# Optimization experiments

Measured on AMD Instinct MI355X. Metric: run time of the kernel, lower is better.

Reference implementation:

```python
import jax, jax.numpy as jnp
import numpy as np

N = 50000        # nodes
E = 800000       # edges
F_IN = 128       # num_features
H = 256          # hidden_dim
B = 128          # number of graphs (batch_size)
NUM_CLASSES = 10
SCALE = 3        # (r-1)*Lev+1 = 3
NNZ = 1200000    # nnz of multiscale wavelet transform matrix [SCALE*N, N]


def setup_inputs() -> dict:
    key = jax.random.key(0)
    ks = jax.random.split(key, 16)
    x = jax.random.normal(ks[0], (N, F_IN), jnp.float32)
    edge_index = jax.random.randint(ks[1], (2, E), 0, N)
    batch = jnp.sort(jax.random.randint(ks[2], (N,), 0, B))
    d = jax.random.normal(ks[3], (NNZ,), jnp.float32) * 0.1
    rows = jax.random.randint(ks[4], (NNZ,), 0, SCALE * N)
    cols = jax.random.randint(ks[5], (NNZ,), 0, N)
    d_index = jnp.stack([rows, cols])

    def lin(k, fi, fo):
        return jax.random.normal(k, (fi, fo), jnp.float32) * (1.0 / np.sqrt(fi))

    return {
        "x": x,
        "W1": lin(ks[6], F_IN, H), "b1": jnp.zeros((H,), jnp.float32),
        "W2": lin(ks[7], H, H),    "b2": jnp.zeros((H,), jnp.float32),
        "W3": lin(ks[8], H, H),    "b3": jnp.zeros((H,), jnp.float32),
        "fc1_w": lin(ks[9], SCALE * H, H),  "fc1_b": jnp.zeros((H,), jnp.float32),
        "fc2_w": lin(ks[10], H, H // 2),    "fc2_b": jnp.zeros((H // 2,), jnp.float32),
        "fc3_w": lin(ks[11], H // 2, NUM_CLASSES), "fc3_b": jnp.zeros((NUM_CLASSES,), jnp.float32),
        "d": d,
        "edge_index": edge_index,
        "batch": batch,
        "d_index": d_index,
    }


def reference(x, W1, b1, W2, b2, W3, b3, fc1_w, fc1_b, fc2_w, fc2_b,
              fc3_w, fc3_b, d, edge_index, batch, d_index):
    # --- GCN normalization (PyG GCNConv: add self-loops, sym norm) ---
    loops = jnp.arange(N, dtype=edge_index.dtype)
    src = jnp.concatenate([edge_index[0], loops])
    dst = jnp.concatenate([edge_index[1], loops])
    deg = jax.ops.segment_sum(jnp.ones_like(src, jnp.float32), dst, num_segments=N)
    dinv = jax.lax.rsqrt(jnp.maximum(deg, 1.0))  # deg >= 1 due to self-loops
    norm = dinv[src] * dinv[dst]                 # [E+N]

    def gcn(h, W, b):
        m = h @ W                                              # [N, H]
        agg = jax.ops.segment_sum(norm[:, None] * m[src], dst, num_segments=N)
        return agg + b

    h = jax.nn.relu(gcn(x, W1, b1))
    h = jax.nn.relu(gcn(h, W2, b2))
    h = jax.nn.relu(gcn(h, W3, b3))

    # --- MultiScale wavelet transform + per-graph pooling ---
    # sparse [SCALE*N, N] matmul: xt = T @ h
    xt = jax.ops.segment_sum(d[:, None] * h[d_index[1]], d_index[0],
                             num_segments=SCALE * N)           # [SCALE*N, H]
    # pool per (scale, graph): segment id = scale*B + graph_id
    seg = (jnp.arange(SCALE)[:, None] * B + batch[None, :]).reshape(-1)
    pooled = jax.ops.segment_sum(xt, seg, num_segments=SCALE * B)
    pooled = pooled.reshape(SCALE, B, H).transpose(1, 0, 2).reshape(B, SCALE * H)

    # --- FC head (dropout is identity in eval) ---
    z = jax.nn.relu(pooled @ fc1_w + fc1_b)
    z = jax.nn.relu(z @ fc2_w + fc2_b)
    return jax.nn.log_softmax(z @ fc3_w + fc3_b, axis=-1)      # [B, NUM_CLASSES]
```

## Files before the change

### kernel.cpp

```cpp
#include <hip/hip_runtime.h>
#include <hip/hip_bf16.h>

#define GN 50000
#define GE 800000
#define FIN 128
#define GH 256
#define GB 128
#define NCLS 10
#define GSCALE 3
#define GNNZ 1200000
#define NSEG (GSCALE * GB)
#define PAD 16

__global__ __launch_bounds__(256) void deg_count_kernel(const int* __restrict__ dst,
                                                        int* __restrict__ deg) {
  int i = blockIdx.x * 256 + threadIdx.x;
  if (i < GE) atomicAdd(&deg[dst[i]], 1);
}

__global__ __launch_bounds__(256) void dinv_kernel(const int* __restrict__ deg,
                                                   float* __restrict__ dinv) {
  int i = blockIdx.x * 256 + threadIdx.x;
  if (i < GN) dinv[i] = 1.0f / sqrtf((float)(deg[i] + 1));
}

__global__ __launch_bounds__(256) void scan1_kernel(const int* __restrict__ in,
                                                    int* __restrict__ out,
                                                    int* __restrict__ btot, int n) {
  __shared__ int sh[256];
  int b = blockIdx.x, tid = threadIdx.x;
  int i = b * 256 + tid;
  int v = (i < n) ? in[i] : 0;
  sh[tid] = v;
  __syncthreads();
  for (int ofs = 1; ofs < 256; ofs <<= 1) {
    int t = (tid >= ofs) ? sh[tid - ofs] : 0;
    __syncthreads();
    sh[tid] += t;
    __syncthreads();
  }
  if (i < n) out[i] = sh[tid] - v;
  if (tid == 255) btot[b] = sh[255];
}

__global__ __launch_bounds__(256) void scan2_kernel(int* __restrict__ btot, int nb) {
  __shared__ int sh[256];
  int tid = threadIdx.x;
  int v = (tid < nb) ? btot[tid] : 0;
  sh[tid] = v;
  __syncthreads();
  for (int ofs = 1; ofs < 256; ofs <<= 1) {
    int t = (tid >= ofs) ? sh[tid - ofs] : 0;
    __syncthreads();
    sh[tid] += t;
    __syncthreads();
  }
  if (tid < nb) btot[tid] = sh[tid] - v;
}

__global__ __launch_bounds__(256) void scan3_kernel(int* __restrict__ out,
                                                    const int* __restrict__ btot,
                                                    int n, int total) {
  int b = blockIdx.x, tid = threadIdx.x;
  int i = b * 256 + tid;
  if (i < n) out[i] += btot[b];
  if (i == 0) out[n] = total;
}

__global__ __launch_bounds__(256) void exscan_strided_kernel(const int* __restrict__ in,
                                                             int* __restrict__ out,
                                                             int n, int stride) {
  __shared__ int sh[256];
  __shared__ int carry;
  int tid = threadIdx.x;
  if (tid == 0) carry = 0;
  __syncthreads();
  for (int base = 0; base < n; base += 256) {
    int i = base + tid;
    int v = (i < n) ? in[(size_t)i * stride] : 0;
    sh[tid] = v;
    __syncthreads();
    for (int ofs = 1; ofs < 256; ofs <<= 1) {
      int t = (tid >= ofs) ? sh[tid - ofs] : 0;
      __syncthreads();
      sh[tid] += t;
      __syncthreads();
    }
    if (i < n) out[i] = carry + sh[tid] - v;
    int total = sh[255];
    __syncthreads();
    if (tid == 0) carry += total;
    __syncthreads();
  }
  if (tid == 0) out[n] = carry;
}

__global__ __launch_bounds__(256) void csr_fill_kernel(const int* __restrict__ src,
                                                       const int* __restrict__ dst,
                                                       int* __restrict__ cur,
                                                       int* __restrict__ csr_src) {
  int i = blockIdx.x * 256 + threadIdx.x;
  if (i < GE) {
    int j = atomicAdd(&cur[dst[i]], 1);
    csr_src[j] = src[i];
  }
}

__device__ __forceinline__ int seg_of(int row, const int* __restrict__ batch) {
  int sc = row / GN;
  int node = row - sc * GN;
  return sc * GB + batch[node];
}

__global__ __launch_bounds__(256) void seg_cnt_kernel(const int* __restrict__ rows,
                                                      const int* __restrict__ batch,
                                                      int* __restrict__ scnt_p) {
  int i = blockIdx.x * 256 + threadIdx.x;
  if (i < GNNZ) atomicAdd(&scnt_p[(size_t)seg_of(rows[i], batch) * PAD], 1);
}

__global__ __launch_bounds__(256) void scur_init_kernel(const int* __restrict__ soff,
                                                        int* __restrict__ scur_p) {
  int s = blockIdx.x * 256 + threadIdx.x;
  if (s < NSEG) scur_p[(size_t)s * PAD] = soff[s];
}

__global__ __launch_bounds__(256) void seg_fill_kernel(const int* __restrict__ rows,
                                                       const int* __restrict__ cols,
                                                       const float* __restrict__ d,
                                                       const int* __restrict__ batch,
                                                       int* __restrict__ scur_p,
                                                       int* __restrict__ scol,
                                                       float* __restrict__ sd) {
  int i = blockIdx.x * 256 + threadIdx.x;
  if (i < GNNZ) {
    int j = atomicAdd(&scur_p[(size_t)seg_of(rows[i], batch) * PAD], 1);
    scol[j] = cols[i];
    sd[j] = d[i];
  }
}

template <int K>
__global__ __launch_bounds__(256) void gemm_kernel(const float* __restrict__ A,
                                                   const float* __restrict__ W,
                                                   float* __restrict__ C, int M) {
  __shared__ float As[16][64];
  __shared__ float Bs[16][64];
  int tid = threadIdx.x;
  int col0 = blockIdx.x * 64;
  int row0 = blockIdx.y * 64;
  float acc[4][4] = {};
  int ar = tid >> 2, akq = tid & 3;
  int bkr = tid >> 4, bcq = tid & 15;
  int ty = tid >> 4, tx = tid & 15;
  for (int kk = 0; kk < K; kk += 16) {
    int arow = row0 + ar;
    if (arow >= M) arow = M - 1;
    float4 av = *(const float4*)&A[(size_t)arow * K + kk + akq * 4];
    float4 bv = *(const float4*)&W[(size_t)(kk + bkr) * GH + col0 + bcq * 4];
    __syncthreads();
    As[akq * 4 + 0][ar] = av.x;
    As[akq * 4 + 1][ar] = av.y;
    As[akq * 4 + 2][ar] = av.z;
    As[akq * 4 + 3][ar] = av.w;
    *(float4*)&Bs[bkr][bcq * 4] = bv;
    __syncthreads();
#pragma unroll
    for (int k = 0; k < 16; ++k) {
      float4 a = *(const float4*)&As[k][ty * 4];
      float4 b = *(const float4*)&Bs[k][tx * 4];
      acc[0][0] += a.x * b.x; acc[0][1] += a.x * b.y; acc[0][2] += a.x * b.z; acc[0][3] += a.x * b.w;
      acc[1][0] += a.y * b.x; acc[1][1] += a.y * b.y; acc[1][2] += a.y * b.z; acc[1][3] += a.y * b.w;
      acc[2][0] += a.z * b.x; acc[2][1] += a.z * b.y; acc[2][2] += a.z * b.z; acc[2][3] += a.z * b.w;
      acc[3][0] += a.w * b.x; acc[3][1] += a.w * b.y; acc[3][2] += a.w * b.z; acc[3][3] += a.w * b.w;
    }
  }
#pragma unroll
  for (int i = 0; i < 4; ++i) {
    int r = row0 + ty * 4 + i;
    if (r < M) {
      float4 v = make_float4(acc[i][0], acc[i][1], acc[i][2], acc[i][3]);
      *(float4*)&C[(size_t)r * GH + col0 + tx * 4] = v;
    }
  }
}

__global__ __launch_bounds__(256) void agg_kernel(const float* __restrict__ m,
                                                  const float* __restrict__ dinv,
                                                  const int* __restrict__ off,
                                                  const int* __restrict__ srcs,
                                                  const float* __restrict__ bias,
                                                  float* __restrict__ out) {
  int node = blockIdx.x * 4 + (threadIdx.x >> 6);
  if (node >= GN) return;
  int lane = threadIdx.x & 63;
  float4 acc = *(const float4*)&bias[lane * 4];
  float di = dinv[node];
  float w0 = di * di;
  float4 mv = *(const float4*)&m[(size_t)node * GH + lane * 4];
  acc.x += w0 * mv.x; acc.y += w0 * mv.y; acc.z += w0 * mv.z; acc.w += w0 * mv.w;
  int e0 = off[node], e1 = off[node + 1];
  for (int e = e0; e < e1; ++e) {
    int s = srcs[e];
    float w = di * dinv[s];
    float4 v = *(const float4*)&m[(size_t)s * GH + lane * 4];
    acc.x += w * v.x; acc.y += w * v.y; acc.z += w * v.z; acc.w += w * v.w;
  }
  acc.x = fmaxf(acc.x, 0.f); acc.y = fmaxf(acc.y, 0.f);
  acc.z = fmaxf(acc.z, 0.f); acc.w = fmaxf(acc.w, 0.f);
  *(float4*)&out[(size_t)node * GH + lane * 4] = acc;
}

__global__ __launch_bounds__(256) void pooled_kernel(const float* __restrict__ h,
                                                     const int* __restrict__ soff,
                                                     const int* __restrict__ scol,
                                                     const float* __restrict__ sd,
                                                     float* __restrict__ pooled) {
  __shared__ int lcol[256];
  __shared__ float ld[256];
  int seg = blockIdx.x;
  int j0 = soff[seg], j1 = soff[seg + 1];
  int cnt = j1 - j0;
  int nparts = gridDim.y;
  int per = (cnt + nparts - 1) / nparts;
  int s = j0 + blockIdx.y * per;
  int e = s + per;
  if (e > j1) e = j1;
  int tid = threadIdx.x;
  float acc = 0.f;
  for (int base = s; base < e; base += 256) {
    int nload = e - base;
    if (nload > 256) nload = 256;
    __syncthreads();
    if (tid < nload) {
      lcol[tid] = scol[base + tid];
      ld[tid] = sd[base + tid];
    }
    __syncthreads();
    for (int t = 0; t < nload; ++t) {
      acc += ld[t] * h[(size_t)lcol[t] * GH + tid];
    }
  }
  atomicAdd(&pooled[(size_t)seg * GH + tid], acc);
}

__global__ __launch_bounds__(256) void fc1_kernel(const float* __restrict__ pooled,
                                                  const float* __restrict__ w,
                                                  const float* __restrict__ b,
                                                  float* __restrict__ z1) {
  __shared__ float vin[GSCALE * GH];
  int g = blockIdx.x, tid = threadIdx.x;
#pragma unroll
  for (int it = 0; it < GSCALE; ++it)
    vin[it * GH + tid] = pooled[(size_t)(it * GB + g) * GH + tid];
  __syncthreads();
  float acc = b[tid];
  for (int j = 0; j < GSCALE * GH; ++j) acc += vin[j] * w[(size_t)j * GH + tid];
  z1[(size_t)g * GH + tid] = fmaxf(acc, 0.f);
}

__global__ __launch_bounds__(128) void fc2_kernel(const float* __restrict__ z1,
                                                  const float* __restrict__ w,
                                                  const float* __restrict__ b,
                                                  float* __restrict__ z2) {
  __shared__ float vin[GH];
  int g = blockIdx.x, tid = threadIdx.x;
  vin[tid] = z1[(size_t)g * GH + tid];
  vin[128 + tid] = z1[(size_t)g * GH + 128 + tid];
  __syncthreads();
  float acc = b[tid];
  for (int j = 0; j < GH; ++j) acc += vin[j] * w[(size_t)j * 128 + tid];
  z2[(size_t)g * 128 + tid] = fmaxf(acc, 0.f);
}

__global__ __launch_bounds__(128) void fc3_kernel(const float* __restrict__ z2,
                                                  const float* __restrict__ w,
                                                  const float* __restrict__ b,
                                                  float* __restrict__ out) {
  int g = threadIdx.x;
  float logit[NCLS];
#pragma unroll
  for (int o = 0; o < NCLS; ++o) logit[o] = b[o];
  for (int k = 0; k < 128; ++k) {
    float zv = z2[(size_t)g * 128 + k];
#pragma unroll
    for (int o = 0; o < NCLS; ++o) logit[o] += zv * w[k * NCLS + o];
  }
  float mx = logit[0];
#pragma unroll
  for (int o = 1; o < NCLS; ++o) mx = fmaxf(mx, logit[o]);
  float lse = 0.f;
#pragma unroll
  for (int o = 0; o < NCLS; ++o) lse += expf(logit[o] - mx);
  lse = logf(lse);
#pragma unroll
  for (int o = 0; o < NCLS; ++o) out[(size_t)g * NCLS + o] = logit[o] - mx - lse;
}

static inline size_t alignup(size_t x) { return (x + 1023) & ~(size_t)1023; }

extern "C" void kernel_launch(void* const* d_in, const int* in_sizes, int n_in,
                              void* d_out, int out_size, void* d_ws, size_t ws_size,
                              hipStream_t stream) {
  const float* x      = (const float*)d_in[0];
  const float* W1     = (const float*)d_in[1];
  const float* b1     = (const float*)d_in[2];
  const float* W2     = (const float*)d_in[3];
  const float* b2     = (const float*)d_in[4];
  const float* W3     = (const float*)d_in[5];
  const float* b3     = (const float*)d_in[6];
  const float* fc1w   = (const float*)d_in[7];
  const float* fc1b   = (const float*)d_in[8];
  const float* fc2w   = (const float*)d_in[9];
  const float* fc2b   = (const float*)d_in[10];
  const float* fc3w   = (const float*)d_in[11];
  const float* fc3b   = (const float*)d_in[12];
  const float* dval   = (const float*)d_in[13];
  const int* eidx     = (const int*)d_in[14];
  const int* batch    = (const int*)d_in[15];
  const int* didx     = (const int*)d_in[16];
  float* out          = (float*)d_out;

  const int* esrc = eidx;
  const int* edst = eidx + GE;
  const int* nzrow = didx;
  const int* nzcol = didx + GNNZ;

  char* ws = (char*)d_ws;
  size_t o = 0;
  auto take = [&](size_t bytes) { char* p = ws + o; o += alignup(bytes); return p; };
  int*   deg     = (int*)take(GN * 4);
  int*   off     = (int*)take((GN + 1) * 4);
  int*   cur     = (int*)take(GN * 4);
  int*   btot    = (int*)take(256 * 4);
  float* dinv    = (float*)take(GN * 4);
  int*   csr_src = (int*)take(GE * 4);
  int*   scnt_p  = (int*)take(NSEG * PAD * 4);
  int*   soff    = (int*)take((NSEG + 1) * 4);
  int*   scur_p  = (int*)take(NSEG * PAD * 4);
  int*   scol    = (int*)take(GNNZ * 4);
  float* sd      = (float*)take(GNNZ * 4);
  float* mbuf    = (float*)take((size_t)GN * GH * 4);
  float* hA      = (float*)take((size_t)GN * GH * 4);
  float* hB      = (float*)take((size_t)GN * GH * 4);
  float* pooled  = (float*)take((size_t)NSEG * GH * 4);
  float* z1      = (float*)take((size_t)GB * GH * 4);
  float* z2      = (float*)take((size_t)GB * 128 * 4);
  (void)ws_size; (void)n_in; (void)in_sizes; (void)out_size;

  const int NB = (GN + 255) / 256;

  hipMemsetAsync(deg, 0, GN * 4, stream);
  hipMemsetAsync(scnt_p, 0, NSEG * PAD * 4, stream);
  hipMemsetAsync(pooled, 0, (size_t)NSEG * GH * 4, stream);

  deg_count_kernel<<<GE / 256, 256, 0, stream>>>(edst, deg);
  dinv_kernel<<<NB, 256, 0, stream>>>(deg, dinv);
  scan1_kernel<<<NB, 256, 0, stream>>>(deg, off, btot, GN);
  scan2_kernel<<<1, 256, 0, stream>>>(btot, NB);
  scan3_kernel<<<NB, 256, 0, stream>>>(off, btot, GN, GE);
  hipMemcpyAsync(cur, off, GN * 4, hipMemcpyDeviceToDevice, stream);
  csr_fill_kernel<<<GE / 256, 256, 0, stream>>>(esrc, edst, cur, csr_src);

  seg_cnt_kernel<<<(GNNZ + 255) / 256, 256, 0, stream>>>(nzrow, batch, scnt_p);
  exscan_strided_kernel<<<1, 256, 0, stream>>>(scnt_p, soff, NSEG, PAD);
  scur_init_kernel<<<(NSEG + 255) / 256, 256, 0, stream>>>(soff, scur_p);
  seg_fill_kernel<<<(GNNZ + 255) / 256, 256, 0, stream>>>(nzrow, nzcol, dval, batch,
                                                          scur_p, scol, sd);

  dim3 ggrid(GH / 64, (GN + 63) / 64);
  gemm_kernel<FIN><<<ggrid, 256, 0, stream>>>(x, W1, mbuf, GN);
  agg_kernel<<<(GN + 3) / 4, 256, 0, stream>>>(mbuf, dinv, off, csr_src, b1, hA);
  gemm_kernel<GH><<<ggrid, 256, 0, stream>>>(hA, W2, mbuf, GN);
  agg_kernel<<<(GN + 3) / 4, 256, 0, stream>>>(mbuf, dinv, off, csr_src, b2, hB);
  gemm_kernel<GH><<<ggrid, 256, 0, stream>>>(hB, W3, mbuf, GN);
  agg_kernel<<<(GN + 3) / 4, 256, 0, stream>>>(mbuf, dinv, off, csr_src, b3, hA);

  pooled_kernel<<<dim3(NSEG, 8), 256, 0, stream>>>(hA, soff, scol, sd, pooled);

  fc1_kernel<<<GB, 256, 0, stream>>>(pooled, fc1w, fc1b, z1);
  fc2_kernel<<<GB, 128, 0, stream>>>(z1, fc2w, fc2b, z2);
  fc3_kernel<<<1, 128, 0, stream>>>(z2, fc3w, fc3b, out);
}
```

Before: 1.152 ms.

## Restructure wavelet pooling as column-sorted scatter into LDS segment accumulators

The sparse wavelet-transform nonzeros are now sorted by column (node) instead of by output segment. Each block owns a node chunk and a 32-wide feature slice, reads each h row slice once, and scatters d*h into a shared-memory accumulator over all 384 segments. Per-chunk partials are written into the reused GEMM buffer and summed by a separate reduction kernel. This replaces the old per-segment gather of random h rows and its contended global atomics, at the cost of LDS atomics and an extra reduction pass. The GCN aggregation loop is also unrolled by two edges to raise memory-level parallelism.

```diff
diff --git a/kernel.cpp b/kernel.cpp
--- a/kernel.cpp
+++ b/kernel.cpp
@@ -10,7 +10,11 @@
 #define GSCALE 3
 #define GNNZ 1200000
 #define NSEG (GSCALE * GB)
-#define PAD 16
+
+#define SLW 32
+#define NSLICE (GH / SLW)
+#define NCHUNK 64
+#define CPC ((GN + NCHUNK - 1) / NCHUNK)
 
 __global__ __launch_bounds__(256) void deg_count_kernel(const int* __restrict__ dst,
                                                         int* __restrict__ deg) {
@@ -67,34 +71,6 @@
   if (i == 0) out[n] = total;
 }
 
-__global__ __launch_bounds__(256) void exscan_strided_kernel(const int* __restrict__ in,
-                                                             int* __restrict__ out,
-                                                             int n, int stride) {
-  __shared__ int sh[256];
-  __shared__ int carry;
-  int tid = threadIdx.x;
-  if (tid == 0) carry = 0;
-  __syncthreads();
-  for (int base = 0; base < n; base += 256) {
-    int i = base + tid;
-    int v = (i < n) ? in[(size_t)i * stride] : 0;
-    sh[tid] = v;
-    __syncthreads();
-    for (int ofs = 1; ofs < 256; ofs <<= 1) {
-      int t = (tid >= ofs) ? sh[tid - ofs] : 0;
-      __syncthreads();
-      sh[tid] += t;
-      __syncthreads();
-    }
-    if (i < n) out[i] = carry + sh[tid] - v;
-    int total = sh[255];
-    __syncthreads();
-    if (tid == 0) carry += total;
-    __syncthreads();
-  }
-  if (tid == 0) out[n] = carry;
-}
-
 __global__ __launch_bounds__(256) void csr_fill_kernel(const int* __restrict__ src,
                                                        const int* __restrict__ dst,
                                                        int* __restrict__ cur,
@@ -112,31 +88,24 @@
   return sc * GB + batch[node];
 }
 
-__global__ __launch_bounds__(256) void seg_cnt_kernel(const int* __restrict__ rows,
-                                                      const int* __restrict__ batch,
-                                                      int* __restrict__ scnt_p) {
-  int i = blockIdx.x * 256 + threadIdx.x;
-  if (i < GNNZ) atomicAdd(&scnt_p[(size_t)seg_of(rows[i], batch) * PAD], 1);
-}
-
-__global__ __launch_bounds__(256) void scur_init_kernel(const int* __restrict__ soff,
-                                                        int* __restrict__ scur_p) {
-  int s = blockIdx.x * 256 + threadIdx.x;
-  if (s < NSEG) scur_p[(size_t)s * PAD] = soff[s];
-}
-
-__global__ __launch_bounds__(256) void seg_fill_kernel(const int* __restrict__ rows,
+__global__ __launch_bounds__(256) void col_cnt_kernel(const int* __restrict__ cols,
+                                                      int* __restrict__ ccnt) {
+  int i = blockIdx.x * 256 + threadIdx.x;
+  if (i < GNNZ) atomicAdd(&ccnt[cols[i]], 1);
+}
+
+__global__ __launch_bounds__(256) void col_fill_kernel(const int* __restrict__ rows,
                                                        const int* __restrict__ cols,
                                                        const float* __restrict__ d,
                                                        const int* __restrict__ batch,
-                                                       int* __restrict__ scur_p,
-                                                       int* __restrict__ scol,
-                                                       float* __restrict__ sd) {
+                                                       int* __restrict__ ccur,
+                                                       int* __restrict__ bseg,
+                                                       float* __restrict__ bd) {
   int i = blockIdx.x * 256 + threadIdx.x;
   if (i < GNNZ) {
-    int j = atomicAdd(&scur_p[(size_t)seg_of(rows[i], batch) * PAD], 1);
-    scol[j] = cols[i];
-    sd[j] = d[i];
+    int j = atomicAdd(&ccur[cols[i]], 1);
+    bseg[j] = seg_of(rows[i], batch);
+    bd[j] = d[i];
   }
 }
 
@@ -200,7 +169,19 @@
   float4 mv = *(const float4*)&m[(size_t)node * GH + lane * 4];
   acc.x += w0 * mv.x; acc.y += w0 * mv.y; acc.z += w0 * mv.z; acc.w += w0 * mv.w;
   int e0 = off[node], e1 = off[node + 1];
-  for (int e = e0; e < e1; ++e) {
+  int e = e0;
+  for (; e + 2 <= e1; e += 2) {
+    int s0 = srcs[e], s1 = srcs[e + 1];
+    float w0a = di * dinv[s0];
+    float w1a = di * dinv[s1];
+    float4 v0 = *(const float4*)&m[(size_t)s0 * GH + lane * 4];
+    float4 v1 = *(const float4*)&m[(size_t)s1 * GH + lane * 4];
+    acc.x += w0a * v0.x + w1a * v1.x;
+    acc.y += w0a * v0.y + w1a * v1.y;
+    acc.z += w0a * v0.z + w1a * v1.z;
+    acc.w += w0a * v0.w + w1a * v1.w;
+  }
+  if (e < e1) {
     int s = srcs[e];
     float w = di * dinv[s];
     float4 v = *(const float4*)&m[(size_t)s * GH + lane * 4];
@@ -211,37 +192,54 @@
   *(float4*)&out[(size_t)node * GH + lane * 4] = acc;
 }
 
-__global__ __launch_bounds__(256) void pooled_kernel(const float* __restrict__ h,
-                                                     const int* __restrict__ soff,
-                                                     const int* __restrict__ scol,
-                                                     const float* __restrict__ sd,
-                                                     float* __restrict__ pooled) {
-  __shared__ int lcol[256];
-  __shared__ float ld[256];
+__global__ __launch_bounds__(256) void pooled2_kernel(const float* __restrict__ h,
+                                                      const int* __restrict__ coff,
+                                                      const int* __restrict__ bseg,
+                                                      const float* __restrict__ bd,
+                                                      float* __restrict__ pp) {
+  __shared__ float acc[NSEG * SLW];
+  int tid = threadIdx.x;
+  int chunk = blockIdx.x, slice = blockIdx.y;
+#pragma unroll
+  for (int t = tid; t < NSEG * SLW; t += 256) acc[t] = 0.f;
+  __syncthreads();
+
+  int wid = tid >> 6;
+  int lane = tid & 63;
+  int sub = lane >> 5;
+  int f = lane & 31;
+  int c0base = chunk * CPC;
+  int cend = c0base + CPC;
+  if (cend > GN) cend = GN;
+  for (int c0 = c0base + wid * 2; c0 < cend; c0 += 8) {
+    int c = c0 + sub;
+    bool valid = c < cend;
+    float hv = valid ? h[(size_t)c * GH + slice * SLW + f] : 0.f;
+    int p0 = valid ? coff[c] : 0;
+    int p1 = valid ? coff[c + 1] : 0;
+    for (int p = p0; p < p1; ++p) {
+      int s = bseg[p];
+      float dv = bd[p];
+      atomicAdd(&acc[s * SLW + f], dv * hv);
+    }
+  }
+  __syncthreads();
+  float* dst = &pp[((size_t)slice * NCHUNK + chunk) * (NSEG * SLW)];
+#pragma unroll
+  for (int t = tid; t < NSEG * SLW; t += 256) dst[t] = acc[t];
+}
+
+__global__ __launch_bounds__(256) void pool_reduce_kernel(const float* __restrict__ pp,
+                                                          float* __restrict__ pooled) {
   int seg = blockIdx.x;
-  int j0 = soff[seg], j1 = soff[seg + 1];
-  int cnt = j1 - j0;
-  int nparts = gridDim.y;
-  int per = (cnt + nparts - 1) / nparts;
-  int s = j0 + blockIdx.y * per;
-  int e = s + per;
-  if (e > j1) e = j1;
   int tid = threadIdx.x;
-  float acc = 0.f;
-  for (int base = s; base < e; base += 256) {
-    int nload = e - base;
-    if (nload > 256) nload = 256;
-    __syncthreads();
-    if (tid < nload) {
-      lcol[tid] = scol[base + tid];
-      ld[tid] = sd[base + tid];
-    }
-    __syncthreads();
-    for (int t = 0; t < nload; ++t) {
-      acc += ld[t] * h[(size_t)lcol[t] * GH + tid];
-    }
-  }
-  atomicAdd(&pooled[(size_t)seg * GH + tid], acc);
+  int slice = tid >> 5;
+  int f = tid & 31;
+  float v = 0.f;
+  for (int ch = 0; ch < NCHUNK; ++ch) {
+    v += pp[((size_t)slice * NCHUNK + ch) * (NSEG * SLW) + seg * SLW + f];
+  }
+  pooled[(size_t)seg * GH + tid] = v;
 }
 
 __global__ __launch_bounds__(256) void fc1_kernel(const float* __restrict__ pooled,
@@ -335,24 +333,24 @@
   int*   btot    = (int*)take(256 * 4);
   float* dinv    = (float*)take(GN * 4);
   int*   csr_src = (int*)take(GE * 4);
-  int*   scnt_p  = (int*)take(NSEG * PAD * 4);
-  int*   soff    = (int*)take((NSEG + 1) * 4);
-  int*   scur_p  = (int*)take(NSEG * PAD * 4);
-  int*   scol    = (int*)take(GNNZ * 4);
-  float* sd      = (float*)take(GNNZ * 4);
+  int*   ccnt    = (int*)take(GN * 4);
+  int*   coff    = (int*)take((GN + 1) * 4);
+  int*   ccur    = (int*)take(GN * 4);
+  int*   bseg    = (int*)take((size_t)GNNZ * 4);
+  float* bd      = (float*)take((size_t)GNNZ * 4);
   float* mbuf    = (float*)take((size_t)GN * GH * 4);
   float* hA      = (float*)take((size_t)GN * GH * 4);
   float* hB      = (float*)take((size_t)GN * GH * 4);
   float* pooled  = (float*)take((size_t)NSEG * GH * 4);
   float* z1      = (float*)take((size_t)GB * GH * 4);
   float* z2      = (float*)take((size_t)GB * 128 * 4);
+  float* pp      = mbuf;
   (void)ws_size; (void)n_in; (void)in_sizes; (void)out_size;
 
   const int NB = (GN + 255) / 256;
 
   hipMemsetAsync(deg, 0, GN * 4, stream);
-  hipMemsetAsync(scnt_p, 0, NSEG * PAD * 4, stream);
-  hipMemsetAsync(pooled, 0, (size_t)NSEG * GH * 4, stream);
+  hipMemsetAsync(ccnt, 0, GN * 4, stream);
 
   deg_count_kernel<<<GE / 256, 256, 0, stream>>>(edst, deg);
   dinv_kernel<<<NB, 256, 0, stream>>>(deg, dinv);
@@ -362,11 +360,13 @@
   hipMemcpyAsync(cur, off, GN * 4, hipMemcpyDeviceToDevice, stream);
   csr_fill_kernel<<<GE / 256, 256, 0, stream>>>(esrc, edst, cur, csr_src);
 
-  seg_cnt_kernel<<<(GNNZ + 255) / 256, 256, 0, stream>>>(nzrow, batch, scnt_p);
-  exscan_strided_kernel<<<1, 256, 0, stream>>>(scnt_p, soff, NSEG, PAD);
-  scur_init_kernel<<<(NSEG + 255) / 256, 256, 0, stream>>>(soff, scur_p);
-  seg_fill_kernel<<<(GNNZ + 255) / 256, 256, 0, stream>>>(nzrow, nzcol, dval, batch,
-                                                          scur_p, scol, sd);
+  col_cnt_kernel<<<(GNNZ + 255) / 256, 256, 0, stream>>>(nzcol, ccnt);
+  scan1_kernel<<<NB, 256, 0, stream>>>(ccnt, coff, btot, GN);
+  scan2_kernel<<<1, 256, 0, stream>>>(btot, NB);
+  scan3_kernel<<<NB, 256, 0, stream>>>(coff, btot, GN, GNNZ);
+  hipMemcpyAsync(ccur, coff, GN * 4, hipMemcpyDeviceToDevice, stream);
+  col_fill_kernel<<<(GNNZ + 255) / 256, 256, 0, stream>>>(nzrow, nzcol, dval, batch,
+                                                          ccur, bseg, bd);
 
   dim3 ggrid(GH / 64, (GN + 63) / 64);
   gemm_kernel<FIN><<<ggrid, 256, 0, stream>>>(x, W1, mbuf, GN);
@@ -376,7 +376,8 @@
   gemm_kernel<GH><<<ggrid, 256, 0, stream>>>(hB, W3, mbuf, GN);
   agg_kernel<<<(GN + 3) / 4, 256, 0, stream>>>(mbuf, dinv, off, csr_src, b3, hA);
 
-  pooled_kernel<<<dim3(NSEG, 8), 256, 0, stream>>>(hA, soff, scol, sd, pooled);
+  pooled2_kernel<<<dim3(NCHUNK, NSLICE), 256, 0, stream>>>(hA, coff, bseg, bd, pp);
+  pool_reduce_kernel<<<NSEG, 256, 0, stream>>>(pp, pooled);
 
   fc1_kernel<<<GB, 256, 0, stream>>>(pooled, fc1w, fc1b, z1);
   fc2_kernel<<<GB, 128, 0, stream>>>(z1, fc2w, fc2b, z2);
```

After: 2.521 ms. +118.8%, slower.
